# Optimization experiments

Measured on AMD Instinct MI355X. Metric: run time of the kernel, lower is better.

Reference implementation:

```python
import jax, jax.numpy as jnp
import numpy as np

NEG_SLOPE = 0.2  # PyG GATv2Conv default negative_slope
NUM_GRAPHS = 512


def _gatv2_layer(x, Wl, Wr, att, bias, src, dst, n):
    # GATv2: e_ij = att . LeakyReLU(Wl x_j + Wr x_i); softmax over incoming edges of i
    xl = x @ Wl                      # [N, H] source transform
    xr = x @ Wr                      # [N, H] target transform
    e = jax.nn.leaky_relu(xl[src] + xr[dst], NEG_SLOPE)  # [E, H]
    logits = e @ att                 # [E]
    m = jax.ops.segment_max(logits, dst, num_segments=n)
    a = jnp.exp(logits - m[dst])
    denom = jax.ops.segment_sum(a, dst, num_segments=n)
    a = a / denom[dst]               # segment softmax (every node has a self loop)
    out = jax.ops.segment_sum(a[:, None] * xl[src], dst, num_segments=n)
    return out + bias


def setup_inputs() -> dict:
    key = jax.random.key(0)
    ks = jax.random.split(key, 12)
    N, E, Cin, H, Cout = 100000, 3200000, 19, 32, 4
    x = jax.random.normal(ks[0], (N, Cin), dtype=jnp.float32)
    edge_index = jax.random.randint(ks[1], (2, E), 0, N, dtype=jnp.int64)
    batch = jnp.sort(jax.random.randint(ks[2], (N,), 0, NUM_GRAPHS, dtype=jnp.int64))
    s = 0.1
    return {
        "x": x,
        "edge_index": edge_index,
        "batch": batch,
        "Wl1": jax.random.normal(ks[3], (Cin, H), dtype=jnp.float32) * s,
        "Wr1": jax.random.normal(ks[4], (Cin, H), dtype=jnp.float32) * s,
        "att1": jax.random.normal(ks[5], (H,), dtype=jnp.float32) * s,
        "b1": jnp.zeros((H,), dtype=jnp.float32),
        "Wl2": jax.random.normal(ks[6], (H, H), dtype=jnp.float32) * s,
        "Wr2": jax.random.normal(ks[7], (H, H), dtype=jnp.float32) * s,
        "att2": jax.random.normal(ks[8], (H,), dtype=jnp.float32) * s,
        "b2": jnp.zeros((H,), dtype=jnp.float32),
        "Wlin": jax.random.normal(ks[9], (H, Cout), dtype=jnp.float32) * s,
        "blin": jnp.zeros((Cout,), dtype=jnp.float32),
    }


def reference(x, edge_index, batch, Wl1, Wr1, att1, b1, Wl2, Wr2, att2, b2, Wlin, blin):
    n = x.shape[0]
    loops = jnp.arange(n, dtype=edge_index.dtype)  # add_self_loops=True (PyG default)
    src = jnp.concatenate([edge_index[0], loops])
    dst = jnp.concatenate([edge_index[1], loops])
    h = jax.nn.relu(_gatv2_layer(x, Wl1, Wr1, att1, b1, src, dst, n))
    h = jax.nn.relu(_gatv2_layer(h, Wl2, Wr2, att2, b2, src, dst, n))
    # global_mean_pool over graph ids
    sums = jax.ops.segment_sum(h, batch, num_segments=NUM_GRAPHS)
    cnt = jax.ops.segment_sum(jnp.ones((n,), h.dtype), batch, num_segments=NUM_GRAPHS)
    features = sums / jnp.maximum(cnt, 1.0)[:, None]
    logits = features @ Wlin + blin
    return logits, features
```

## Files before the change

### kernel.cpp

```cpp
#include <hip/hip_runtime.h>
#include <cstdint>
#include <cstddef>

#define WG 256
#define NPB 256
#define NPB_SHIFT 8
#define CAP 9216
#define BIN_CHUNK 4096
#define LIN_NPB 128

typedef _Float16 half4 __attribute__((ext_vector_type(4)));


__device__ __forceinline__ void lin_block(const float* __restrict__ x,
                                          const float* __restrict__ Wl,
                                          const float* __restrict__ Wr,
                                          _Float16* __restrict__ xl,
                                          _Float16* __restrict__ xr,
                                          long base_n, int N, int Cin, int t,
                                          float* sl, float* sr,
                                          float* sx0, float* sx1) {
    for (int i = t; i < Cin * 32; i += 512) { sl[i] = Wl[i]; sr[i] = Wr[i]; }
    {
        int cnt0 = (int)min((long)16, (long)N - base_n);
        if (cnt0 > 0)
            for (int i = t; i < cnt0 * Cin; i += 512)
                sx0[i] = x[base_n * Cin + i];
    }
    __syncthreads();
#pragma unroll 1
    for (int g = 0; g < LIN_NPB / 16; g++) {
        long n0 = base_n + (long)g * 16;
        if (n0 >= N) break;
        float* scur = (g & 1) ? sx1 : sx0;
        float* snxt = (g & 1) ? sx0 : sx1;
        long n1 = n0 + 16;
        if (g < LIN_NPB / 16 - 1 && n1 < N) {
            int cnt1 = (int)min((long)16, (long)N - n1);
            for (int i = t; i < cnt1 * Cin; i += 512)
                snxt[i] = x[n1 * Cin + i];
        }
        int cnt = (int)min((long)16, (long)N - n0);
        int n = t >> 5, h = t & 31;
        if (n < cnt) {
            float al = 0.f, ar = 0.f;
            for (int k = 0; k < Cin; k++) {
                float xv = scur[n * Cin + k];
                al = fmaf(xv, sl[k * 32 + h], al);
                ar = fmaf(xv, sr[k * 32 + h], ar);
            }
            xl[(n0 + n) * 32 + h] = (_Float16)al;
            xr[(n0 + n) * 32 + h] = (_Float16)ar;
        }
        __syncthreads();
    }
}

__global__ __launch_bounds__(512) void k_front(
        const int* __restrict__ esrc, const int* __restrict__ edst,
        int* __restrict__ gcnt, unsigned* __restrict__ staging,
        int E, int NB) {
    __shared__ unsigned sval[BIN_CHUNK];
    __shared__ unsigned short sbkt[BIN_CHUNK];
    __shared__ int hist[512];
    __shared__ int cursor[512];
    __shared__ int gbase[512];
    __shared__ int wtot[8];
    __shared__ int stotal;

    int t = threadIdx.x;

    hist[t] = 0;
    __syncthreads();
    long base = (long)blockIdx.x * BIN_CHUNK;
    int vb[BIN_CHUNK / 512];
    unsigned vv[BIN_CHUNK / 512];
#pragma unroll
    for (int k = 0; k < BIN_CHUNK / 512; k++) {
        long e = base + k * 512 + t;
        int b = -1; unsigned v = 0;
        if (e < E) {
            int d = edst[e];
            b = d >> NPB_SHIFT;
            v = ((unsigned)esrc[e] << NPB_SHIFT) | (unsigned)(d & (NPB - 1));
            atomicAdd(&hist[b], 1);
        }
        vb[k] = b; vv[k] = v;
    }
    __syncthreads();
    int lane = t & 63, wvq = t >> 6;
    int c = hist[t];
    int v = c;
#pragma unroll
    for (int off = 1; off < 64; off <<= 1) {
        int u = __shfl_up(v, off);
        if (lane >= off) v += u;
    }
    if (lane == 63) wtot[wvq] = v;
    __syncthreads();
    int add = 0;
#pragma unroll
    for (int wq = 0; wq < 8; wq++) add += (wq < wvq) ? wtot[wq] : 0;
    int incl = v + add;
    int st = incl - c;
    cursor[t] = st;
    if (t == 511) stotal = incl;
    int wb = 0;
    if (t < NB && c > 0) wb = atomicAdd(&gcnt[t], c);
    gbase[t] = wb + t * CAP - st;
    __syncthreads();
#pragma unroll
    for (int k = 0; k < BIN_CHUNK / 512; k++) {
        int b = vb[k];
        if (b >= 0) {
            int r = atomicAdd(&cursor[b], 1);
            sval[r] = vv[k];
            sbkt[r] = (unsigned short)b;
        }
    }
    __syncthreads();
    int total = stotal;
    for (int j = t; j < total; j += 512) {
        int b = sbkt[j];
        int addr = gbase[b] + j;
        if (addr < (b + 1) * CAP)
            staging[addr] = sval[j];
    }
}

__global__ __launch_bounds__(512) void k_bucket(
        const unsigned* __restrict__ staging, const int* __restrict__ gcnt,
        int* __restrict__ offsets, int* __restrict__ csr_src,
        int N, int NB,
        const float* __restrict__ x, const float* __restrict__ Wl,
        const float* __restrict__ Wr, _Float16* __restrict__ xl,
        _Float16* __restrict__ xr, int Cin, int linBlocks,
        const int* __restrict__ batch, int* __restrict__ gstart, int G,
        int stBlocks, const float* __restrict__ W2l,
        const float* __restrict__ W2r, float* __restrict__ w2t) {
    __shared__ unsigned sslab[CAP];
    __shared__ int hist[NPB];
    __shared__ int cur[NPB];
    __shared__ int wtot[8];
    int t = threadIdx.x;

    if (blockIdx.x < (unsigned)NB) {
        int b = blockIdx.x;
        int lane = t & 63, wv = t >> 6;

        int a = 0;
        for (int j = t; j < b; j += 512)
            a += min(gcnt[j], CAP) + min(NPB, N - j * NPB);
#pragma unroll
        for (int off = 1; off < 64; off <<= 1) a += __shfl_xor(a, off);
        if (lane == 0) wtot[wv] = a;
        if (t < NPB) hist[t] = 0;
        __syncthreads();
        int bbase = wtot[0] + wtot[1] + wtot[2] + wtot[3]
                  + wtot[4] + wtot[5] + wtot[6] + wtot[7];

        int cnt = min(gcnt[b], CAP);
        const unsigned* slab = staging + (long)b * CAP;
        for (int j = t; j < cnt; j += 512) {
            unsigned e = slab[j];
            sslab[j] = e;
            atomicAdd(&hist[e & (NPB - 1)], 1);
        }
        if (b == NB - 1 && t == 0)
            offsets[N] = bbase + cnt + min(NPB, N - b * NPB);
        __syncthreads();

        int node = b * NPB + t;
        int c = 0, v = 0;
        if (t < NPB) {
            c = (node < N) ? hist[t] + 1 : 0;
            v = c;
#pragma unroll
            for (int off = 1; off < 64; off <<= 1) {
                int u = __shfl_up(v, off);
                if (lane >= off) v += u;
            }
            if (lane == 63) wtot[wv] = v;
        }
        __syncthreads();
        if (t < NPB) {
            int add = (wv >= 1 ? wtot[0] : 0) + (wv >= 2 ? wtot[1] : 0)
                    + (wv >= 3 ? wtot[2] : 0);
            int o = bbase + (v + add) - c;
            if (node < N) {
                offsets[node] = o;
                csr_src[o] = node;
                cur[t] = o + 1;
            }
        }
        __syncthreads();
        for (int j = t; j < cnt; j += 512) {
            unsigned e = sslab[j];
            int p = atomicAdd(&cur[e & (NPB - 1)], 1);
            csr_src[p] = (int)(e >> NPB_SHIFT);
        }
    } else if (blockIdx.x < (unsigned)(NB + linBlocks)) {
        float* sl  = (float*)sslab;
        float* sr  = (float*)sslab + 1024;
        float* sx0 = (float*)sslab + 2048;
        float* sx1 = sx0 + 16 * Cin;
        long base_n = (long)(blockIdx.x - NB) * LIN_NPB;
        lin_block(x, Wl, Wr, xl, xr, base_n, N, Cin, t, sl, sr, sx0, sx1);
    } else if (blockIdx.x < (unsigned)(NB + linBlocks + stBlocks)) {
        int g = (blockIdx.x - NB - linBlocks) * 512 + t;
        if (g <= G) {
            int lo = 0, hi = N;
            while (lo < hi) {
                int mid = (lo + hi) >> 1;
                if (batch[mid] < g) lo = mid + 1; else hi = mid;
            }
            gstart[g] = lo;
        }
    } else {
        for (int i = t; i < 1024; i += 512) {
            int k = i >> 5, c = i & 31;
            int q = (k >> 2) * 128 + c * 4 + (k & 3);
            w2t[q]        = W2l[i];
            w2t[1024 + q] = W2r[i];
        }
    }
}

template <int MODE>
__global__ __launch_bounds__(WG) void k_gat(
        const _Float16* __restrict__ xl, const _Float16* __restrict__ xr,
        const int* __restrict__ offsets, const int* __restrict__ csr,
        const float* __restrict__ att, const float* __restrict__ bias,
        int N,
        const float* __restrict__ w2t,
        _Float16* __restrict__ oxl, _Float16* __restrict__ oxr,
        float* __restrict__ out) {
    __shared__ float sO[WG / 64][2][32];
    int lane = threadIdx.x & 63;
    int wv = threadIdx.x >> 6;
    int wid = blockIdx.x * (WG / 64) + wv;
    int iA = wid * 2;
    if (iA >= N) return;
    int iB = iA + 1;
    int e8 = lane >> 3;
    int hq = lane & 7;
    unsigned hq8 = (unsigned)hq << 3;

    const char* xlb = (const char*)xl;
    const char* csrb = (const char*)csr;

    int startA = offsets[iA], endA = offsets[iA + 1];
    int startB = 0, endB = 0;
    if (iB < N) { startB = endA; endB = offsets[iB + 1]; }

    float4 att4 = *(const float4*)(att + hq * 4);
    const float L2E = 1.4426950408889634f;
    att4.x *= L2E; att4.y *= L2E; att4.z *= L2E; att4.w *= L2E;

    const _Float16 ns = (_Float16)0.2f;
    half4 hzero = {(_Float16)0.f, (_Float16)0.f, (_Float16)0.f, (_Float16)0.f};

    half4 xrA = *(const half4*)(xr + (long)iA * 32 + hq * 4);
    half4 xrB = hzero;
    if (iB < N) xrB = *(const half4*)(xr + (long)iB * 32 + hq * 4);

    float denomA = 0.f, denomB = 0.f;
    float4 accA = {0.f, 0.f, 0.f, 0.f};
    float4 accB = {0.f, 0.f, 0.f, 0.f};

    int itA = (endA - startA + 7) >> 3;
    int itB = (endB - startB + 7) >> 3;
    int iters = max(itA, itB);

    int pA = startA + e8, pB = startB + e8;
    int sA = -1, sB = -1;
    if (pA < endA) sA = *(const int*)(csrb + ((unsigned)pA << 2));
    if (pB < endB) sB = *(const int*)(csrb + ((unsigned)pB << 2));

    for (int it = 0; it < iters; ++it) {
        half4 xa = hzero;
        half4 xb = hzero;
        if (sA >= 0) xa = *(const half4*)(xlb + (((unsigned)sA << 6) | hq8));
        if (sB >= 0) xb = *(const half4*)(xlb + (((unsigned)sB << 6) | hq8));
        pA += 8; pB += 8;
        int sA2 = -1, sB2 = -1;
        if (pA < endA) sA2 = *(const int*)(csrb + ((unsigned)pA << 2));
        if (pB < endB) sB2 = *(const int*)(csrb + ((unsigned)pB << 2));

        {
            half4 s = xa + xrA;
            half4 m = s * ns;
            half4 tt = __builtin_elementwise_max(s, m);
            float l = fmaf((float)tt[0], att4.x,
                      fmaf((float)tt[1], att4.y,
                      fmaf((float)tt[2], att4.z,
                           (float)tt[3] * att4.w)));
            l += __shfl_xor(l, 1);
            l += __shfl_xor(l, 2);
            l += __shfl_xor(l, 4);
            float wA = __builtin_amdgcn_exp2f(l);
            wA = (sA >= 0) ? wA : 0.f;
            denomA += wA;
            accA.x = fmaf(wA, (float)xa[0], accA.x);
            accA.y = fmaf(wA, (float)xa[1], accA.y);
            accA.z = fmaf(wA, (float)xa[2], accA.z);
            accA.w = fmaf(wA, (float)xa[3], accA.w);
        }
        {
            half4 s = xb + xrB;
            half4 m = s * ns;
            half4 tt = __builtin_elementwise_max(s, m);
            float l = fmaf((float)tt[0], att4.x,
                      fmaf((float)tt[1], att4.y,
                      fmaf((float)tt[2], att4.z,
                           (float)tt[3] * att4.w)));
            l += __shfl_xor(l, 1);
            l += __shfl_xor(l, 2);
            l += __shfl_xor(l, 4);
            float wB = __builtin_amdgcn_exp2f(l);
            wB = (sB >= 0) ? wB : 0.f;
            denomB += wB;
            accB.x = fmaf(wB, (float)xb[0], accB.x);
            accB.y = fmaf(wB, (float)xb[1], accB.y);
            accB.z = fmaf(wB, (float)xb[2], accB.z);
            accB.w = fmaf(wB, (float)xb[3], accB.w);
        }
        sA = sA2; sB = sB2;
    }

    denomA += __shfl_xor(denomA, 8); denomA += __shfl_xor(denomA, 16); denomA += __shfl_xor(denomA, 32);
    denomB += __shfl_xor(denomB, 8); denomB += __shfl_xor(denomB, 16); denomB += __shfl_xor(denomB, 32);
    accA.x += __shfl_xor(accA.x, 8); accA.x += __shfl_xor(accA.x, 16); accA.x += __shfl_xor(accA.x, 32);
    accA.y += __shfl_xor(accA.y, 8); accA.y += __shfl_xor(accA.y, 16); accA.y += __shfl_xor(accA.y, 32);
    accA.z += __shfl_xor(accA.z, 8); accA.z += __shfl_xor(accA.z, 16); accA.z += __shfl_xor(accA.z, 32);
    accA.w += __shfl_xor(accA.w, 8); accA.w += __shfl_xor(accA.w, 16); accA.w += __shfl_xor(accA.w, 32);
    accB.x += __shfl_xor(accB.x, 8); accB.x += __shfl_xor(accB.x, 16); accB.x += __shfl_xor(accB.x, 32);
    accB.y += __shfl_xor(accB.y, 8); accB.y += __shfl_xor(accB.y, 16); accB.y += __shfl_xor(accB.y, 32);
    accB.z += __shfl_xor(accB.z, 8); accB.z += __shfl_xor(accB.z, 16); accB.z += __shfl_xor(accB.z, 32);
    accB.w += __shfl_xor(accB.w, 8); accB.w += __shfl_xor(accB.w, 16); accB.w += __shfl_xor(accB.w, 32);

    const float4 b4 = *(const float4*)(bias + hq * 4);

    if (MODE == 0) {
        float invA = 1.0f / denomA;
        float4 oA;
        oA.x = fmaxf(fmaf(accA.x, invA, b4.x), 0.f);
        oA.y = fmaxf(fmaf(accA.y, invA, b4.y), 0.f);
        oA.z = fmaxf(fmaf(accA.z, invA, b4.z), 0.f);
        oA.w = fmaxf(fmaf(accA.w, invA, b4.w), 0.f);
        float4 oB = {0.f, 0.f, 0.f, 0.f};
        if (iB < N) {
            float invB = 1.0f / denomB;
            oB.x = fmaxf(fmaf(accB.x, invB, b4.x), 0.f);
            oB.y = fmaxf(fmaf(accB.y, invB, b4.y), 0.f);
            oB.z = fmaxf(fmaf(accB.z, invB, b4.z), 0.f);
            oB.w = fmaxf(fmaf(accB.w, invB, b4.w), 0.f);
        }
        if (lane < 8) {
            *(float4*)&sO[wv][0][hq * 4] = oA;
        } else if (lane < 16) {
            *(float4*)&sO[wv][1][hq * 4] = oB;
        }
        __builtin_amdgcn_wave_barrier();
        int hcol = lane & 31;
        int nrow = lane >> 5;
        const float* row = &sO[wv][nrow][0];
        const float* wlq = w2t + hcol * 4;
        const float* wrq = w2t + 1024 + hcol * 4;
        float al = 0.f, ar = 0.f;
#pragma unroll
        for (int kb = 0; kb < 8; kb++) {
            float4 r4 = *(const float4*)(row + kb * 4);
            float4 wl4 = *(const float4*)(wlq + kb * 128);
            float4 wr4 = *(const float4*)(wrq + kb * 128);
            al = fmaf(r4.x, wl4.x, al);
            al = fmaf(r4.y, wl4.y, al);
            al = fmaf(r4.z, wl4.z, al);
            al = fmaf(r4.w, wl4.w, al);
            ar = fmaf(r4.x, wr4.x, ar);
            ar = fmaf(r4.y, wr4.y, ar);
            ar = fmaf(r4.z, wr4.z, ar);
            ar = fmaf(r4.w, wr4.w, ar);
        }
        long nn = nrow ? (long)iB : (long)iA;
        if (!nrow || iB < N) {
            oxl[nn * 32 + hcol] = (_Float16)al;
            oxr[nn * 32 + hcol] = (_Float16)ar;
        }
    } else {
        if (lane < 8) {
            float inv = 1.0f / denomA;
            float4 o;
            o.x = fmaxf(fmaf(accA.x, inv, b4.x), 0.f);
            o.y = fmaxf(fmaf(accA.y, inv, b4.y), 0.f);
            o.z = fmaxf(fmaf(accA.z, inv, b4.z), 0.f);
            o.w = fmaxf(fmaf(accA.w, inv, b4.w), 0.f);
            *(float4*)(out + (long)iA * 32 + hq * 4) = o;
        } else if (lane < 16 && iB < N) {
            float inv = 1.0f / denomB;
            float4 o;
            o.x = fmaxf(fmaf(accB.x, inv, b4.x), 0.f);
            o.y = fmaxf(fmaf(accB.y, inv, b4.y), 0.f);
            o.z = fmaxf(fmaf(accB.z, inv, b4.z), 0.f);
            o.w = fmaxf(fmaf(accB.w, inv, b4.w), 0.f);
            *(float4*)(out + (long)iB * 32 + hq * 4) = o;
        }
    }
}

__global__ __launch_bounds__(WG) void k_pool(const float* __restrict__ h2v,
                                             const int* __restrict__ gstart,
                                             const float* __restrict__ Wlin,
                                             const float* __restrict__ blin,
                                             float* __restrict__ out, int G) {
    __shared__ float red[WG];
    int g = blockIdx.x;
    int t = threadIdx.x;
    int h = t & 31;
    int grp = t >> 5;
    int s = gstart[g], e = gstart[g + 1];
    float acc = 0.f;
    for (int n = s + grp; n < e; n += 8)
        acc += h2v[(long)n * 32 + h];
    red[t] = acc;
    __syncthreads();
    if (grp == 0) {
        float a = red[h] + red[h + 32] + red[h + 64] + red[h + 96]
                + red[h + 128] + red[h + 160] + red[h + 192] + red[h + 224];
        int cnt = e - s;
        float c = (float)(cnt > 1 ? cnt : 1);
        float f = a / c;
        out[G * 4 + g * 32 + h] = f;
        float p0 = f * Wlin[h * 4 + 0];
        float p1 = f * Wlin[h * 4 + 1];
        float p2 = f * Wlin[h * 4 + 2];
        float p3 = f * Wlin[h * 4 + 3];
        for (int off = 1; off < 32; off <<= 1) {
            p0 += __shfl_xor(p0, off);
            p1 += __shfl_xor(p1, off);
            p2 += __shfl_xor(p2, off);
            p3 += __shfl_xor(p3, off);
        }
        if (h == 0) {
            out[g * 4 + 0] = p0 + blin[0];
            out[g * 4 + 1] = p1 + blin[1];
            out[g * 4 + 2] = p2 + blin[2];
            out[g * 4 + 3] = p3 + blin[3];
        }
    }
}

extern "C" void kernel_launch(void* const* d_in, const int* in_sizes, int n_in,
                              void* d_out, int out_size, void* d_ws, size_t ws_size,
                              hipStream_t stream) {
    const float* x    = (const float*)d_in[0];
    const int*   ei   = (const int*)d_in[1];
    const int*   batch= (const int*)d_in[2];
    const float* Wl1  = (const float*)d_in[3];
    const float* Wr1  = (const float*)d_in[4];
    const float* att1 = (const float*)d_in[5];
    const float* b1   = (const float*)d_in[6];
    const float* Wl2  = (const float*)d_in[7];
    const float* Wr2  = (const float*)d_in[8];
    const float* att2 = (const float*)d_in[9];
    const float* b2   = (const float*)d_in[10];
    const float* Wlin = (const float*)d_in[11];
    const float* blin = (const float*)d_in[12];
    float* out = (float*)d_out;

    const int N   = in_sizes[2];
    const int Cin = in_sizes[0] / N;
    const int E   = in_sizes[1] / 2;
    const int G   = out_size / 36;
    const int* src = ei;
    const int* dst = ei + E;
    const int NB  = (N + NPB - 1) >> NPB_SHIFT;

    char* w = (char*)d_ws;
    auto alloc = [&](size_t bytes) {
        char* p = w;
        w += (bytes + 255) & ~(size_t)255;
        return p;
    };
    int* offsets = (int*)alloc((size_t)(N + 1) * 4);
    int* gstart  = (int*)alloc((size_t)(G + 1) * 4);
    int* gcnt    = (int*)alloc((size_t)NB * 4);
    int* csr_src = (int*)alloc((size_t)(E + N) * 4);
    unsigned* staging = (unsigned*)alloc((size_t)NB * CAP * 4);
    float* w2t   = (float*)alloc((size_t)2048 * 4);
    _Float16* xl  = (_Float16*)alloc((size_t)N * 32 * 2);
    _Float16* xr  = (_Float16*)alloc((size_t)N * 32 * 2);
    _Float16* xl2 = (_Float16*)alloc((size_t)N * 32 * 2);
    _Float16* xr2 = (_Float16*)alloc((size_t)N * 32 * 2);
    float* h2v    = (float*)alloc((size_t)N * 32 * 4);

    hipMemsetAsync(gcnt, 0, (size_t)NB * 4, stream);

    int binBlocks = (E + BIN_CHUNK - 1) / BIN_CHUNK;
    int linBlocks = (N + LIN_NPB - 1) / LIN_NPB;
    int stBlocks  = (G + 1 + 511) / 512;

    k_front<<<binBlocks, 512, 0, stream>>>(src, dst, gcnt, staging, E, NB);

    k_bucket<<<NB + linBlocks + stBlocks + 1, 512, 0, stream>>>(
        staging, gcnt, offsets, csr_src, N, NB,
        x, Wl1, Wr1, xl, xr, Cin, linBlocks,
        batch, gstart, G, stBlocks, Wl2, Wr2, w2t);

    int waves = (N + 1) / 2;
    int gat_grid = (waves + 3) / 4;

    k_gat<0><<<gat_grid, WG, 0, stream>>>(xl, xr, offsets, csr_src, att1, b1,
                                          N, w2t, xl2, xr2, nullptr);

    k_gat<1><<<gat_grid, WG, 0, stream>>>(xl2, xr2, offsets, csr_src, att2, b2,
                                          N, nullptr, nullptr, nullptr, h2v);

    k_pool<<<G, WG, 0, stream>>>(h2v, gstart, Wlin, blin, out, G);
}
```

Measured before the change: 267.7 us.

## Process one node per wave with 16 edges × 4 lanes of half8 loads

The GAT aggregation kernel moves from two nodes per wave (8 edges × 8 lanes, half4 loads) to one node per wave with 16 edges in flight, each handled by 4 lanes loading 8 halves (16 bytes). Each lane does more arithmetic per gather and the logit reduction needs fewer shuffles. The fused layer-2 linear transform now splits Wl and Wr across the two half-waves. The grid doubles in wave count, and nodes with low degree may leave lanes idle because 16 edge slots are processed per iteration.

After: 277.1 us. +3.5%, slower.

```diff
diff --git a/kernel.cpp b/kernel.cpp
--- a/kernel.cpp
+++ b/kernel.cpp
@@ -9,7 +9,7 @@
 #define BIN_CHUNK 4096
 #define LIN_NPB 128
 
-typedef _Float16 half4 __attribute__((ext_vector_type(4)));
+typedef _Float16 half8 __attribute__((ext_vector_type(8)));
 
 
 __device__ __forceinline__ void lin_block(const float* __restrict__ x,
@@ -235,175 +235,122 @@
         const float* __restrict__ w2t,
         _Float16* __restrict__ oxl, _Float16* __restrict__ oxr,
         float* __restrict__ out) {
-    __shared__ float sO[WG / 64][2][32];
+    __shared__ float sO[WG / 64][32];
     int lane = threadIdx.x & 63;
     int wv = threadIdx.x >> 6;
-    int wid = blockIdx.x * (WG / 64) + wv;
-    int iA = wid * 2;
-    if (iA >= N) return;
-    int iB = iA + 1;
-    int e8 = lane >> 3;
-    int hq = lane & 7;
-    unsigned hq8 = (unsigned)hq << 3;
+    int i = blockIdx.x * (WG / 64) + wv;
+    if (i >= N) return;
+    int e16 = lane >> 2;
+    int q = lane & 3;
+    unsigned qb = (unsigned)q << 4;
 
     const char* xlb = (const char*)xl;
     const char* csrb = (const char*)csr;
 
-    int startA = offsets[iA], endA = offsets[iA + 1];
-    int startB = 0, endB = 0;
-    if (iB < N) { startB = endA; endB = offsets[iB + 1]; }
-
-    float4 att4 = *(const float4*)(att + hq * 4);
+    int start = offsets[i], end = offsets[i + 1];
+
     const float L2E = 1.4426950408889634f;
-    att4.x *= L2E; att4.y *= L2E; att4.z *= L2E; att4.w *= L2E;
+    float4 a0 = *(const float4*)(att + q * 8);
+    float4 a1 = *(const float4*)(att + q * 8 + 4);
+    a0.x *= L2E; a0.y *= L2E; a0.z *= L2E; a0.w *= L2E;
+    a1.x *= L2E; a1.y *= L2E; a1.z *= L2E; a1.w *= L2E;
 
     const _Float16 ns = (_Float16)0.2f;
-    half4 hzero = {(_Float16)0.f, (_Float16)0.f, (_Float16)0.f, (_Float16)0.f};
-
-    half4 xrA = *(const half4*)(xr + (long)iA * 32 + hq * 4);
-    half4 xrB = hzero;
-    if (iB < N) xrB = *(const half4*)(xr + (long)iB * 32 + hq * 4);
-
-    float denomA = 0.f, denomB = 0.f;
-    float4 accA = {0.f, 0.f, 0.f, 0.f};
-    float4 accB = {0.f, 0.f, 0.f, 0.f};
-
-    int itA = (endA - startA + 7) >> 3;
-    int itB = (endB - startB + 7) >> 3;
-    int iters = max(itA, itB);
-
-    int pA = startA + e8, pB = startB + e8;
-    int sA = -1, sB = -1;
-    if (pA < endA) sA = *(const int*)(csrb + ((unsigned)pA << 2));
-    if (pB < endB) sB = *(const int*)(csrb + ((unsigned)pB << 2));
+    half8 hzero = {(_Float16)0.f, (_Float16)0.f, (_Float16)0.f, (_Float16)0.f,
+                   (_Float16)0.f, (_Float16)0.f, (_Float16)0.f, (_Float16)0.f};
+
+    half8 xr8 = *(const half8*)((const char*)xr + ((long)i << 6) + qb);
+
+    float denom = 0.f;
+    float4 acc0 = {0.f, 0.f, 0.f, 0.f};
+    float4 acc1 = {0.f, 0.f, 0.f, 0.f};
+
+    int iters = (end - start + 15) >> 4;
+
+    int p = start + e16;
+    int s = -1;
+    if (p < end) s = *(const int*)(csrb + ((unsigned)p << 2));
 
     for (int it = 0; it < iters; ++it) {
-        half4 xa = hzero;
-        half4 xb = hzero;
-        if (sA >= 0) xa = *(const half4*)(xlb + (((unsigned)sA << 6) | hq8));
-        if (sB >= 0) xb = *(const half4*)(xlb + (((unsigned)sB << 6) | hq8));
-        pA += 8; pB += 8;
-        int sA2 = -1, sB2 = -1;
-        if (pA < endA) sA2 = *(const int*)(csrb + ((unsigned)pA << 2));
-        if (pB < endB) sB2 = *(const int*)(csrb + ((unsigned)pB << 2));
-
-        {
-            half4 s = xa + xrA;
-            half4 m = s * ns;
-            half4 tt = __builtin_elementwise_max(s, m);
-            float l = fmaf((float)tt[0], att4.x,
-                      fmaf((float)tt[1], att4.y,
-                      fmaf((float)tt[2], att4.z,
-                           (float)tt[3] * att4.w)));
-            l += __shfl_xor(l, 1);
-            l += __shfl_xor(l, 2);
-            l += __shfl_xor(l, 4);
-            float wA = __builtin_amdgcn_exp2f(l);
-            wA = (sA >= 0) ? wA : 0.f;
-            denomA += wA;
-            accA.x = fmaf(wA, (float)xa[0], accA.x);
-            accA.y = fmaf(wA, (float)xa[1], accA.y);
-            accA.z = fmaf(wA, (float)xa[2], accA.z);
-            accA.w = fmaf(wA, (float)xa[3], accA.w);
-        }
-        {
-            half4 s = xb + xrB;
-            half4 m = s * ns;
-            half4 tt = __builtin_elementwise_max(s, m);
-            float l = fmaf((float)tt[0], att4.x,
-                      fmaf((float)tt[1], att4.y,
-                      fmaf((float)tt[2], att4.z,
-                           (float)tt[3] * att4.w)));
-            l += __shfl_xor(l, 1);
-            l += __shfl_xor(l, 2);
-            l += __shfl_xor(l, 4);
-            float wB = __builtin_amdgcn_exp2f(l);
-            wB = (sB >= 0) ? wB : 0.f;
-            denomB += wB;
-            accB.x = fmaf(wB, (float)xb[0], accB.x);
-            accB.y = fmaf(wB, (float)xb[1], accB.y);
-            accB.z = fmaf(wB, (float)xb[2], accB.z);
-            accB.w = fmaf(wB, (float)xb[3], accB.w);
-        }
-        sA = sA2; sB = sB2;
-    }
-
-    denomA += __shfl_xor(denomA, 8); denomA += __shfl_xor(denomA, 16); denomA += __shfl_xor(denomA, 32);
-    denomB += __shfl_xor(denomB, 8); denomB += __shfl_xor(denomB, 16); denomB += __shfl_xor(denomB, 32);
-    accA.x += __shfl_xor(accA.x, 8); accA.x += __shfl_xor(accA.x, 16); accA.x += __shfl_xor(accA.x, 32);
-    accA.y += __shfl_xor(accA.y, 8); accA.y += __shfl_xor(accA.y, 16); accA.y += __shfl_xor(accA.y, 32);
-    accA.z += __shfl_xor(accA.z, 8); accA.z += __shfl_xor(accA.z, 16); accA.z += __shfl_xor(accA.z, 32);
-    accA.w += __shfl_xor(accA.w, 8); accA.w += __shfl_xor(accA.w, 16); accA.w += __shfl_xor(accA.w, 32);
-    accB.x += __shfl_xor(accB.x, 8); accB.x += __shfl_xor(accB.x, 16); accB.x += __shfl_xor(accB.x, 32);
-    accB.y += __shfl_xor(accB.y, 8); accB.y += __shfl_xor(accB.y, 16); accB.y += __shfl_xor(accB.y, 32);
-    accB.z += __shfl_xor(accB.z, 8); accB.z += __shfl_xor(accB.z, 16); accB.z += __shfl_xor(accB.z, 32);
-    accB.w += __shfl_xor(accB.w, 8); accB.w += __shfl_xor(accB.w, 16); accB.w += __shfl_xor(accB.w, 32);
-
-    const float4 b4 = *(const float4*)(bias + hq * 4);
+        half8 xa = hzero;
+        if (s >= 0) xa = *(const half8*)(xlb + (((unsigned)s << 6) | qb));
+        p += 16;
+        int s2 = -1;
+        if (p < end) s2 = *(const int*)(csrb + ((unsigned)p << 2));
+
+        half8 su = xa + xr8;
+        half8 m = su * ns;
+        half8 tt = __builtin_elementwise_max(su, m);
+        float l = fmaf((float)tt[0], a0.x,
+                  fmaf((float)tt[1], a0.y,
+                  fmaf((float)tt[2], a0.z,
+                  fmaf((float)tt[3], a0.w,
+                  fmaf((float)tt[4], a1.x,
+                  fmaf((float)tt[5], a1.y,
+                  fmaf((float)tt[6], a1.z,
+                       (float)tt[7] * a1.w)))))));
+        l += __shfl_xor(l, 1);
+        l += __shfl_xor(l, 2);
+        float w = __builtin_amdgcn_exp2f(l);
+        w = (s >= 0) ? w : 0.f;
+        denom += w;
+        acc0.x = fmaf(w, (float)xa[0], acc0.x);
+        acc0.y = fmaf(w, (float)xa[1], acc0.y);
+        acc0.z = fmaf(w, (float)xa[2], acc0.z);
+        acc0.w = fmaf(w, (float)xa[3], acc0.w);
+        acc1.x = fmaf(w, (float)xa[4], acc1.x);
+        acc1.y = fmaf(w, (float)xa[5], acc1.y);
+        acc1.z = fmaf(w, (float)xa[6], acc1.z);
+        acc1.w = fmaf(w, (float)xa[7], acc1.w);
+        s = s2;
+    }
+
+#define RED4(v) v += __shfl_xor(v, 4); v += __shfl_xor(v, 8); \
+                v += __shfl_xor(v, 16); v += __shfl_xor(v, 32);
+    RED4(denom)
+    RED4(acc0.x) RED4(acc0.y) RED4(acc0.z) RED4(acc0.w)
+    RED4(acc1.x) RED4(acc1.y) RED4(acc1.z) RED4(acc1.w)
+#undef RED4
+
+    float4 b0 = *(const float4*)(bias + q * 8);
+    float4 b1 = *(const float4*)(bias + q * 8 + 4);
+    float inv = 1.0f / denom;
+    float4 o0, o1;
+    o0.x = fmaxf(fmaf(acc0.x, inv, b0.x), 0.f);
+    o0.y = fmaxf(fmaf(acc0.y, inv, b0.y), 0.f);
+    o0.z = fmaxf(fmaf(acc0.z, inv, b0.z), 0.f);
+    o0.w = fmaxf(fmaf(acc0.w, inv, b0.w), 0.f);
+    o1.x = fmaxf(fmaf(acc1.x, inv, b1.x), 0.f);
+    o1.y = fmaxf(fmaf(acc1.y, inv, b1.y), 0.f);
+    o1.z = fmaxf(fmaf(acc1.z, inv, b1.z), 0.f);
+    o1.w = fmaxf(fmaf(acc1.w, inv, b1.w), 0.f);
 
     if (MODE == 0) {
-        float invA = 1.0f / denomA;
-        float4 oA;
-        oA.x = fmaxf(fmaf(accA.x, invA, b4.x), 0.f);
-        oA.y = fmaxf(fmaf(accA.y, invA, b4.y), 0.f);
-        oA.z = fmaxf(fmaf(accA.z, invA, b4.z), 0.f);
-        oA.w = fmaxf(fmaf(accA.w, invA, b4.w), 0.f);
-        float4 oB = {0.f, 0.f, 0.f, 0.f};
-        if (iB < N) {
-            float invB = 1.0f / denomB;
-            oB.x = fmaxf(fmaf(accB.x, invB, b4.x), 0.f);
-            oB.y = fmaxf(fmaf(accB.y, invB, b4.y), 0.f);
-            oB.z = fmaxf(fmaf(accB.z, invB, b4.z), 0.f);
-            oB.w = fmaxf(fmaf(accB.w, invB, b4.w), 0.f);
-        }
-        if (lane < 8) {
-            *(float4*)&sO[wv][0][hq * 4] = oA;
-        } else if (lane < 16) {
-            *(float4*)&sO[wv][1][hq * 4] = oB;
+        if (lane < 4) {
+            *(float4*)&sO[wv][lane * 8] = o0;
+            *(float4*)&sO[wv][lane * 8 + 4] = o1;
         }
         __builtin_amdgcn_wave_barrier();
-        int hcol = lane & 31;
-        int nrow = lane >> 5;
-        const float* row = &sO[wv][nrow][0];
-        const float* wlq = w2t + hcol * 4;
-        const float* wrq = w2t + 1024 + hcol * 4;
-        float al = 0.f, ar = 0.f;
+        int col = lane & 31;
+        int mat = lane >> 5;
+        const float* wq = w2t + mat * 1024 + col * 4;
+        float a = 0.f;
 #pragma unroll
         for (int kb = 0; kb < 8; kb++) {
-            float4 r4 = *(const float4*)(row + kb * 4);
-            float4 wl4 = *(const float4*)(wlq + kb * 128);
-            float4 wr4 = *(const float4*)(wrq + kb * 128);
-            al = fmaf(r4.x, wl4.x, al);
-            al = fmaf(r4.y, wl4.y, al);
-            al = fmaf(r4.z, wl4.z, al);
-            al = fmaf(r4.w, wl4.w, al);
-            ar = fmaf(r4.x, wr4.x, ar);
-            ar = fmaf(r4.y, wr4.y, ar);
-            ar = fmaf(r4.z, wr4.z, ar);
-            ar = fmaf(r4.w, wr4.w, ar);
-        }
-        long nn = nrow ? (long)iB : (long)iA;
-        if (!nrow || iB < N) {
-            oxl[nn * 32 + hcol] = (_Float16)al;
-            oxr[nn * 32 + hcol] = (_Float16)ar;
-        }
+            float4 r4 = *(const float4*)(&sO[wv][kb * 4]);
+            float4 w4 = *(const float4*)(wq + kb * 128);
+            a = fmaf(r4.x, w4.x, a);
+            a = fmaf(r4.y, w4.y, a);
+            a = fmaf(r4.z, w4.z, a);
+            a = fmaf(r4.w, w4.w, a);
+        }
+        _Float16 hv = (_Float16)a;
+        if (mat) oxr[(long)i * 32 + col] = hv;
+        else     oxl[(long)i * 32 + col] = hv;
     } else {
-        if (lane < 8) {
-            float inv = 1.0f / denomA;
-            float4 o;
-            o.x = fmaxf(fmaf(accA.x, inv, b4.x), 0.f);
-            o.y = fmaxf(fmaf(accA.y, inv, b4.y), 0.f);
-            o.z = fmaxf(fmaf(accA.z, inv, b4.z), 0.f);
-            o.w = fmaxf(fmaf(accA.w, inv, b4.w), 0.f);
-            *(float4*)(out + (long)iA * 32 + hq * 4) = o;
-        } else if (lane < 16 && iB < N) {
-            float inv = 1.0f / denomB;
-            float4 o;
-            o.x = fmaxf(fmaf(accB.x, inv, b4.x), 0.f);
-            o.y = fmaxf(fmaf(accB.y, inv, b4.y), 0.f);
-            o.z = fmaxf(fmaf(accB.z, inv, b4.z), 0.f);
-            o.w = fmaxf(fmaf(accB.w, inv, b4.w), 0.f);
-            *(float4*)(out + (long)iB * 32 + hq * 4) = o;
+        if (lane < 4) {
+            *(float4*)(out + (long)i * 32 + lane * 8) = o0;
+            *(float4*)(out + (long)i * 32 + lane * 8 + 4) = o1;
         }
     }
 }
@@ -507,8 +454,7 @@
         x, Wl1, Wr1, xl, xr, Cin, linBlocks,
         batch, gstart, G, stBlocks, Wl2, Wr2, w2t);
 
-    int waves = (N + 1) / 2;
-    int gat_grid = (waves + 3) / 4;
+    int gat_grid = (N + (WG / 64) - 1) / (WG / 64);
 
     k_gat<0><<<gat_grid, WG, 0, stream>>>(xl, xr, offsets, csr_src, att1, b1,
                                           N, w2t, xl2, xr2, nullptr);
```
